# Performance work log

Measured on AMD Instinct MI355X. Metric: run time of the kernel, lower is better.

Reference implementation:

```python
import jax, jax.numpy as jnp
import numpy as np

B, S, D, H = 2, 2048, 1024, 16
DK = D // H


def setup_inputs() -> dict:
    key = jax.random.key(0)
    ks = jax.random.split(key, 9)
    s = 1.0 / np.sqrt(D)
    return {
        "x": jax.random.normal(ks[0], (B, S, D), dtype=jnp.float32),
        "wq": jax.random.normal(ks[1], (D, D), dtype=jnp.float32) * s,
        "bq": jax.random.normal(ks[2], (D,), dtype=jnp.float32) * 0.01,
        "wk": jax.random.normal(ks[3], (D, D), dtype=jnp.float32) * s,
        "bk": jax.random.normal(ks[4], (D,), dtype=jnp.float32) * 0.01,
        "wv": jax.random.normal(ks[5], (D, D), dtype=jnp.float32) * s,
        "bv": jax.random.normal(ks[6], (D,), dtype=jnp.float32) * 0.01,
        "wo": jax.random.normal(ks[7], (D, D), dtype=jnp.float32) * s,
        "bo": jax.random.normal(ks[8], (D,), dtype=jnp.float32) * 0.01,
    }


def reference(x, wq, bq, wk, bk, wv, bv, wo, bo):
    b, s, d = x.shape
    # Linear layers use torch convention: y = x @ W.T + b
    def proj(w, bias):
        y = jnp.einsum("bsd,ed->bse", x, w) + bias
        return y.reshape(b, s, H, DK).transpose(0, 2, 1, 3)  # (B,H,S,DK)

    q = proj(wq, bq)
    k = proj(wk, bk)
    v = proj(wv, bv)

    # Because each Q-chunk attends to the full K/V with m initialized to -inf,
    # the chunked online-softmax loop is exactly full softmax attention.
    scores = jnp.einsum("bhqd,bhkd->bhqk", q, k) / jnp.sqrt(jnp.float32(DK))
    attn = jax.nn.softmax(scores, axis=-1)
    out = jnp.einsum("bhqk,bhkd->bhqd", attn, v)  # (B,H,S,DK)

    out = out.transpose(0, 2, 1, 3).reshape(b, s, d)
    return jnp.einsum("bsd,ed->bse", out, wo) + bo
```

## Files before the change

### kernel.cpp

```cpp
#include <hip/hip_runtime.h>

typedef __attribute__((ext_vector_type(8))) short s16x8;
typedef __attribute__((ext_vector_type(4))) short s16x4;
typedef __attribute__((ext_vector_type(4))) float f32x4;

#define DEVI static __device__ __forceinline__

DEVI short f2bf(float f) {
  union { float f; unsigned u; } v; v.f = f;
  unsigned u = v.u;
  unsigned r = u + 0x7FFFu + ((u >> 16) & 1u);
  return (short)(r >> 16);
}
DEVI short f2bf_fast(float f) {
  union { float f; unsigned u; } v; v.f = f;
  return (short)((v.u + 0x8000u) >> 16);
}
DEVI float bf2f(short s) {
  union { unsigned u; float f; } v;
  v.u = ((unsigned)(unsigned short)s) << 16;
  return v.f;
}
DEVI f32x4 mfma16(s16x8 a, s16x8 b, f32x4 c) {
  return __builtin_amdgcn_mfma_f32_16x16x32_bf16(a, b, c, 0, 0, 0);
}
DEVI float fexp2(float x) {
#if __has_builtin(__builtin_amdgcn_exp2f)
  return __builtin_amdgcn_exp2f(x);
#else
  float r; asm("v_exp_f32 %0, %1" : "=v"(r) : "v"(x)); return r;
#endif
}
DEVI void gld16(const void* g, void* l) {
  __builtin_amdgcn_global_load_lds(
      (const __attribute__((address_space(1))) void*)g,
      (__attribute__((address_space(3))) void*)l, 16, 0, 0);
}

constexpr int Sc = 2048, Dc = 1024, Hc = 16, DKc = 64;
constexpr int Mc = 4096;

__global__ void detect_ker(const unsigned short* __restrict__ x, int* __restrict__ flag) {
  __shared__ int cnt;
  if (threadIdx.x == 0) cnt = 0;
  __syncthreads();
  int c = 0;
  for (int i = threadIdx.x; i < 4096; i += 256) {
    int e = (x[i] >> 7) & 0xFF;
    if (e >= 140) c++;
  }
  atomicAdd(&cnt, c);
  __syncthreads();
  if (threadIdx.x == 0) *flag = (cnt > 64) ? 1 : 0;
}

__global__ void norm_all(const void* x,
                         const void* w0, const void* w1, const void* w2, const void* w3,
                         const void* b0, const void* b1, const void* b2, const void* b3,
                         short* __restrict__ xdst, short* __restrict__ wdst,
                         float* __restrict__ bdst, const int* __restrict__ flag) {
  const int f = *flag;
  const int blk = blockIdx.x, tid = threadIdx.x;
  if (blk < 8192) {
    if (!f) return;
    const void* src; short* dst; int i;
    if (blk < 4096) {
      i = blk * 256 + tid; src = x; dst = xdst;
    } else {
      int j = (blk - 4096) * 256 + tid;
      int region = j >> 18;
      const void* ws[4] = {w0, w1, w2, w3};
      src = ws[region]; dst = wdst + (size_t)region * 1048576;
      i = j & 262143;
    }
    f32x4 v = ((const f32x4*)src)[i];
    s16x4 o;
#pragma unroll
    for (int j2 = 0; j2 < 4; ++j2) o[j2] = f2bf(v[j2]);
    ((s16x4*)dst)[i] = o;
  } else {
    const void* bs[4] = {b0, b1, b2, b3};
#pragma unroll
    for (int j = 0; j < 16; ++j) {
      int i = tid + j * 256;
      int r = i >> 10, k = i & 1023;
      bdst[i] = f ? ((const float*)bs[r])[k] : bf2f(((const short*)bs[r])[k]);
    }
  }
}

template <int EPI>
__global__ __launch_bounds__(256, 2)
void gemm_bt(const short* __restrict__ Aorig, const short* __restrict__ Acvt,
             const short* __restrict__ W0, const short* __restrict__ W1,
             const short* __restrict__ W2, const short* __restrict__ Wcvt,
             const float* __restrict__ bias_c, short* __restrict__ outQKV,
             short* __restrict__ outV, void* __restrict__ outFinal,
             const int* __restrict__ flag) {
  constexpr int K = Dc, N = Dc;
  const int z = blockIdx.z;
  const int f = *flag;
  const short* A = f ? Acvt : Aorig;
  const short* Wor = (z == 0) ? W0 : (z == 1) ? W1 : W2;
  const short* W = f ? (Wcvt + (size_t)z * 1048576) : Wor;
  const float* bias = bias_c + (size_t)z * N;
  const float oscale = (EPI == 0 && z == 0) ? 0.125f * 1.44269504f : 1.0f;

  __shared__ short lA[128 * 64];
  __shared__ short lB[128 * 64];

  const int tid = threadIdx.x;
  const int lane = tid & 63, wave = tid >> 6;
  const int l16 = lane & 15, quad = lane >> 4;
  const int wm0 = (wave >> 1) * 64, wn0 = (wave & 1) * 64;
  const int m0 = blockIdx.y * 128, n0 = blockIdx.x * 128;
  const int lr = lane >> 3;
  const int cg = ((lane & 7) ^ lr) * 8;
  const int x7 = l16 & 7;

  f32x4 acc[4][4] = {};

  for (int k0 = 0; k0 < K; k0 += 64) {
    __syncthreads();
#pragma unroll
    for (int it = 0; it < 4; ++it) {
      int rbase = wave * 32 + it * 8;
      gld16(&A[(size_t)(m0 + rbase + lr) * K + k0 + cg], &lA[rbase * 64]);
      gld16(&W[(size_t)(n0 + rbase + lr) * K + k0 + cg], &lB[rbase * 64]);
    }
    __syncthreads();
#pragma unroll
    for (int ks = 0; ks < 2; ++ks) {
      const int sw = ((ks * 4 + quad) ^ x7) * 8;
      s16x8 af[4], bfr[4];
#pragma unroll
      for (int i = 0; i < 4; ++i) {
        af[i]  = *(const s16x8*)&lA[(wm0 + i * 16 + l16) * 64 + sw];
        bfr[i] = *(const s16x8*)&lB[(wn0 + i * 16 + l16) * 64 + sw];
      }
#pragma unroll
      for (int mi = 0; mi < 4; ++mi)
#pragma unroll
        for (int ni = 0; ni < 4; ++ni)
          acc[mi][ni] = mfma16(af[mi], bfr[ni], acc[mi][ni]);
    }
  }

  if constexpr (EPI == 0) {
    if (z == 2) {
#pragma unroll
      for (int ni = 0; ni < 4; ++ni) {
        int n = n0 + wn0 + ni * 16 + l16;
        float bv = bias[n];
        int h = (n >> 6) & 15, dk = n & 63;
#pragma unroll
        for (int mi = 0; mi < 4; ++mi) {
          int mbase = m0 + wm0 + mi * 16 + quad * 4;
          int bb = mbase >> 11, s = mbase & 2047;
          s16x4 pk;
#pragma unroll
          for (int r = 0; r < 4; ++r) pk[r] = f2bf(acc[mi][ni][r] + bv);
          *(s16x4*)&outV[(((size_t)(bb * Hc + h)) * DKc + dk) * Sc + s] = pk;
        }
      }
      return;
    }
#pragma unroll
    for (int ni = 0; ni < 4; ++ni) {
      int n = n0 + wn0 + ni * 16 + l16;
      float bv = bias[n];
#pragma unroll
      for (int mi = 0; mi < 4; ++mi) {
#pragma unroll
        for (int r = 0; r < 4; ++r) {
          int m = m0 + wm0 + mi * 16 + quad * 4 + r;
          float v = (acc[mi][ni][r] + bv) * oscale;
          int bb = m >> 11, s = m & 2047, h = n >> 6, dk = n & 63;
          size_t idx = ((((size_t)bb * Hc + h) * Sc) + s) * DKc + dk +
                       (size_t)z * Mc * N;
          outQKV[idx] = f2bf(v);
        }
      }
    }
  } else {
#pragma unroll
    for (int ni = 0; ni < 4; ++ni) {
      int n = n0 + wn0 + ni * 16 + l16;
      float bv = bias[n];
#pragma unroll
      for (int mi = 0; mi < 4; ++mi) {
#pragma unroll
        for (int r = 0; r < 4; ++r) {
          int m = m0 + wm0 + mi * 16 + quad * 4 + r;
          float v = acc[mi][ni][r] + bv;
          if (f) ((float*)outFinal)[(size_t)m * N + n] = v;
          else   ((short*)outFinal)[(size_t)m * N + n] = f2bf(v);
        }
      }
    }
  }
}

__global__ __launch_bounds__(512, 4)
void attn_ker(const short* __restrict__ Q, const short* __restrict__ Kg,
              const short* __restrict__ Vt, short* __restrict__ O) {
  __shared__ short lK[2][64 * 64];
  __shared__ short lV[2][64 * 64];
  __shared__ short lP[8][16][72];

  const int tid = threadIdx.x;
  const int lane = tid & 63, wave = tid >> 6;
  const int l16 = lane & 15, quad = lane >> 4;
  const int lr = lane >> 3;
  const int cg = ((lane & 7) ^ lr) * 8;
  const int x7 = l16 & 7;

  const int bh = blockIdx.x;
  const short* Qb = Q + (size_t)bh * Sc * DKc;
  const short* Kb = Kg + (size_t)bh * Sc * DKc;
  const short* Vb = Vt + (size_t)bh * DKc * Sc;

  const int q0 = blockIdx.y * 128 + wave * 16;

  s16x8 qf[2];
#pragma unroll
  for (int ks = 0; ks < 2; ++ks)
    qf[ks] = *(const s16x8*)&Qb[(size_t)(q0 + l16) * DKc + ks * 32 + quad * 8];

  s16x8 ones = {};
  if (l16 == 0) {
#pragma unroll
    for (int j = 0; j < 8; ++j) ones[j] = (short)0x3F80;
  }
  const f32x4 initC = {-24.f, -24.f, -24.f, -24.f};

  f32x4 oacc[4] = {};
  f32x4 oln = {};

#define STAGE(BUF, KB)                                                          \
  {                                                                             \
    int rbase = wave * 8;                                                       \
    gld16(&Kb[(size_t)((KB) + rbase + lr) * DKc + cg], &lK[BUF][rbase * 64]);   \
    gld16(&Vb[(size_t)(rbase + lr) * Sc + (KB) + cg], &lV[BUF][rbase * 64]);    \
  }

  STAGE(0, 0)

  for (int kt = 0; kt < Sc / 64; ++kt) {
    const int p = kt & 1;
    __syncthreads();
    if (kt + 1 < Sc / 64) STAGE(p ^ 1, (kt + 1) * 64)

    f32x4 sacc[4];
    {
      const int sw0 = (quad ^ x7) * 8;
      s16x8 kf[4];
#pragma unroll
      for (int ni = 0; ni < 4; ++ni)
        kf[ni] = *(const s16x8*)&lK[p][(ni * 16 + l16) * 64 + sw0];
#pragma unroll
      for (int ni = 0; ni < 4; ++ni)
        sacc[ni] = mfma16(qf[0], kf[ni], initC);
    }
    {
      const int sw1 = ((4 + quad) ^ x7) * 8;
      s16x8 kf[4];
#pragma unroll
      for (int ni = 0; ni < 4; ++ni)
        kf[ni] = *(const s16x8*)&lK[p][(ni * 16 + l16) * 64 + sw1];
#pragma unroll
      for (int ni = 0; ni < 4; ++ni)
        sacc[ni] = mfma16(qf[1], kf[ni], sacc[ni]);
    }

#pragma unroll
    for (int r = 0; r < 4; ++r) {
      int row = quad * 4 + r;
#pragma unroll
      for (int ni = 0; ni < 4; ++ni)
        lP[wave][row][ni * 16 + l16] = f2bf_fast(fexp2(sacc[ni][r]));
    }

    s16x8 vf[2][4];
#pragma unroll
    for (int ks = 0; ks < 2; ++ks) {
      const int sw = ((ks * 4 + quad) ^ x7) * 8;
#pragma unroll
      for (int ni = 0; ni < 4; ++ni)
        vf[ks][ni] = *(const s16x8*)&lV[p][(ni * 16 + l16) * 64 + sw];
    }

    __builtin_amdgcn_s_waitcnt(0xc07f);

    s16x8 pf[2];
#pragma unroll
    for (int ks = 0; ks < 2; ++ks)
      pf[ks] = *(const s16x8*)&lP[wave][l16][ks * 32 + quad * 8];

#pragma unroll
    for (int ks = 0; ks < 2; ++ks) {
#pragma unroll
      for (int ni = 0; ni < 4; ++ni)
        oacc[ni] = mfma16(pf[ks], vf[ks][ni], oacc[ni]);
      oln = mfma16(pf[ks], ones, oln);
    }
  }
#undef STAGE

  const int bb = bh >> 4, h = bh & 15;
#pragma unroll
  for (int r = 0; r < 4; ++r) {
    float l = __shfl(oln[r], lane & 48);
    float inv = 1.0f / l;
    int srow = q0 + quad * 4 + r;
#pragma unroll
    for (int ni = 0; ni < 4; ++ni) {
      int col = h * DKc + ni * 16 + l16;
      O[((size_t)(bb * Sc + srow)) * Dc + col] = f2bf(oacc[ni][r] * inv);
    }
  }
}

extern "C" void kernel_launch(void* const* d_in, const int* in_sizes, int n_in,
                              void* d_out, int out_size, void* d_ws, size_t ws_size,
                              hipStream_t stream) {
  const void* x  = d_in[0];
  const void* wq = d_in[1]; const void* bq = d_in[2];
  const void* wk = d_in[3]; const void* bk = d_in[4];
  const void* wv = d_in[5]; const void* bv = d_in[6];
  const void* wo = d_in[7]; const void* bo = d_in[8];

  char* wsb = (char*)d_ws;
  int*   flag = (int*)wsb;
  short* x_c  = (short*)(wsb + 1024);
  short* w_c  = x_c + (size_t)4 * 1024 * 1024;
  float* b_c  = (float*)(wsb + 1024 + 16 * 1024 * 1024);
  short* Qc   = (short*)(wsb + 1024 + 16 * 1024 * 1024 + 16384);
  short* Kc   = Qc + (size_t)4 * 1024 * 1024;
  short* Vtc  = Kc + (size_t)4 * 1024 * 1024;
  short* Oc   = Vtc + (size_t)4 * 1024 * 1024;

  detect_ker<<<1, 256, 0, stream>>>((const unsigned short*)x, flag);

  norm_all<<<8193, 256, 0, stream>>>(x, wq, wk, wv, wo, bq, bk, bv, bo,
                                     x_c, w_c, b_c, flag);

  gemm_bt<0><<<dim3(8, 32, 3), 256, 0, stream>>>(
      (const short*)x, x_c,
      (const short*)wq, (const short*)wk, (const short*)wv, w_c,
      b_c, Qc, Vtc, nullptr, flag);

  attn_ker<<<dim3(32, 16), 512, 0, stream>>>(Qc, Kc, Vtc, Oc);

  gemm_bt<1><<<dim3(8, 32, 1), 256, 0, stream>>>(
      Oc, Oc,
      (const short*)wo, (const short*)wo, (const short*)wo, w_c + 3 * 1048576,
      b_c + 3 * 1024, nullptr, nullptr, d_out, flag);
}
```

Measured before the change: 204.8 us.

## Keep attention probabilities in registers via shuffles, shrink attn and out-proj tiles

The attention kernel now computes S^T (K as the A operand) so that exp'd probabilities can be packed to bf16 pairs and redistributed with lane shuffles into the PV MFMA operand layout. This removes the per-wave LDS round trip for P and its waitcnt. The attention block is halved to 4 waves with 64 queries each, doubling the grid. The output projection gets its own 64x64-tile GEMM, giving 1024 blocks instead of 256 for better CU fill. The risks are added shuffle and select overhead and less K/V reuse per block.

Result: no change. 205.0 us (+0.1%).

```diff
diff --git a/kernel.cpp b/kernel.cpp
--- a/kernel.cpp
+++ b/kernel.cpp
@@ -11,10 +11,6 @@
   unsigned u = v.u;
   unsigned r = u + 0x7FFFu + ((u >> 16) & 1u);
   return (short)(r >> 16);
-}
-DEVI short f2bf_fast(float f) {
-  union { float f; unsigned u; } v; v.f = f;
-  return (short)((v.u + 0x8000u) >> 16);
 }
 DEVI float bf2f(short s) {
   union { unsigned u; float f; } v;
@@ -30,6 +26,10 @@
 #else
   float r; asm("v_exp_f32 %0, %1" : "=v"(r) : "v"(x)); return r;
 #endif
+}
+DEVI unsigned packbf(float lo, float hi) {
+  union { float f; unsigned u; } a, b; a.f = lo; b.f = hi;
+  return __builtin_amdgcn_perm(b.u + 0x8000u, a.u + 0x8000u, 0x07060302u);
 }
 DEVI void gld16(const void* g, void* l) {
   __builtin_amdgcn_global_load_lds(
@@ -89,14 +89,12 @@
   }
 }
 
-template <int EPI>
 __global__ __launch_bounds__(256, 2)
-void gemm_bt(const short* __restrict__ Aorig, const short* __restrict__ Acvt,
-             const short* __restrict__ W0, const short* __restrict__ W1,
-             const short* __restrict__ W2, const short* __restrict__ Wcvt,
-             const float* __restrict__ bias_c, short* __restrict__ outQKV,
-             short* __restrict__ outV, void* __restrict__ outFinal,
-             const int* __restrict__ flag) {
+void gemm_qkv(const short* __restrict__ Aorig, const short* __restrict__ Acvt,
+              const short* __restrict__ W0, const short* __restrict__ W1,
+              const short* __restrict__ W2, const short* __restrict__ Wcvt,
+              const float* __restrict__ bias_c, short* __restrict__ outQKV,
+              short* __restrict__ outV, const int* __restrict__ flag) {
   constexpr int K = Dc, N = Dc;
   const int z = blockIdx.z;
   const int f = *flag;
@@ -104,7 +102,7 @@
   const short* Wor = (z == 0) ? W0 : (z == 1) ? W1 : W2;
   const short* W = f ? (Wcvt + (size_t)z * 1048576) : Wor;
   const float* bias = bias_c + (size_t)z * N;
-  const float oscale = (EPI == 0 && z == 0) ? 0.125f * 1.44269504f : 1.0f;
+  const float oscale = (z == 0) ? 0.125f * 1.44269504f : 1.0f;
 
   __shared__ short lA[128 * 64];
   __shared__ short lB[128 * 64];
@@ -146,67 +144,53 @@
     }
   }
 
-  if constexpr (EPI == 0) {
-    if (z == 2) {
-#pragma unroll
-      for (int ni = 0; ni < 4; ++ni) {
-        int n = n0 + wn0 + ni * 16 + l16;
-        float bv = bias[n];
-        int h = (n >> 6) & 15, dk = n & 63;
-#pragma unroll
-        for (int mi = 0; mi < 4; ++mi) {
-          int mbase = m0 + wm0 + mi * 16 + quad * 4;
-          int bb = mbase >> 11, s = mbase & 2047;
-          s16x4 pk;
-#pragma unroll
-          for (int r = 0; r < 4; ++r) pk[r] = f2bf(acc[mi][ni][r] + bv);
-          *(s16x4*)&outV[(((size_t)(bb * Hc + h)) * DKc + dk) * Sc + s] = pk;
-        }
-      }
-      return;
-    }
+  if (z == 2) {
 #pragma unroll
     for (int ni = 0; ni < 4; ++ni) {
       int n = n0 + wn0 + ni * 16 + l16;
       float bv = bias[n];
+      int h = (n >> 6) & 15, dk = n & 63;
 #pragma unroll
       for (int mi = 0; mi < 4; ++mi) {
-#pragma unroll
-        for (int r = 0; r < 4; ++r) {
-          int m = m0 + wm0 + mi * 16 + quad * 4 + r;
-          float v = (acc[mi][ni][r] + bv) * oscale;
-          int bb = m >> 11, s = m & 2047, h = n >> 6, dk = n & 63;
-          size_t idx = ((((size_t)bb * Hc + h) * Sc) + s) * DKc + dk +
-                       (size_t)z * Mc * N;
-          outQKV[idx] = f2bf(v);
-        }
+        int mbase = m0 + wm0 + mi * 16 + quad * 4;
+        int bb = mbase >> 11, s = mbase & 2047;
+        s16x4 pk;
+#pragma unroll
+        for (int r = 0; r < 4; ++r) pk[r] = f2bf(acc[mi][ni][r] + bv);
+        *(s16x4*)&outV[(((size_t)(bb * Hc + h)) * DKc + dk) * Sc + s] = pk;
       }
     }
-  } else {
-#pragma unroll
-    for (int ni = 0; ni < 4; ++ni) {
-      int n = n0 + wn0 + ni * 16 + l16;
-      float bv = bias[n];
-#pragma unroll
-      for (int mi = 0; mi < 4; ++mi) {
-#pragma unroll
-        for (int r = 0; r < 4; ++r) {
-          int m = m0 + wm0 + mi * 16 + quad * 4 + r;
-          float v = acc[mi][ni][r] + bv;
-          if (f) ((float*)outFinal)[(size_t)m * N + n] = v;
-          else   ((short*)outFinal)[(size_t)m * N + n] = f2bf(v);
-        }
+    return;
+  }
+#pragma unroll
+  for (int ni = 0; ni < 4; ++ni) {
+    int n = n0 + wn0 + ni * 16 + l16;
+    float bv = bias[n];
+#pragma unroll
+    for (int mi = 0; mi < 4; ++mi) {
+#pragma unroll
+      for (int r = 0; r < 4; ++r) {
+        int m = m0 + wm0 + mi * 16 + quad * 4 + r;
+        float v = (acc[mi][ni][r] + bv) * oscale;
+        int bb = m >> 11, s = m & 2047, h = n >> 6, dk = n & 63;
+        size_t idx = ((((size_t)bb * Hc + h) * Sc) + s) * DKc + dk +
+                     (size_t)z * Mc * N;
+        outQKV[idx] = f2bf(v);
       }
     }
   }
 }
 
-__global__ __launch_bounds__(512, 4)
-void attn_ker(const short* __restrict__ Q, const short* __restrict__ Kg,
-              const short* __restrict__ Vt, short* __restrict__ O) {
-  __shared__ short lK[2][64 * 64];
-  __shared__ short lV[2][64 * 64];
-  __shared__ short lP[8][16][72];
+__global__ __launch_bounds__(256, 4)
+void gemm_out(const short* __restrict__ A, const short* __restrict__ Worig,
+              const short* __restrict__ Wcvt, const float* __restrict__ bias,
+              void* __restrict__ out, const int* __restrict__ flag) {
+  constexpr int K = Dc, N = Dc;
+  const int f = *flag;
+  const short* W = f ? Wcvt : Worig;
+
+  __shared__ short lA[64 * 64];
+  __shared__ short lB[64 * 64];
 
   const int tid = threadIdx.x;
   const int lane = tid & 63, wave = tid >> 6;
@@ -214,13 +198,73 @@
   const int lr = lane >> 3;
   const int cg = ((lane & 7) ^ lr) * 8;
   const int x7 = l16 & 7;
+  const int wm0 = (wave >> 1) * 32, wn0 = (wave & 1) * 32;
+  const int m0 = blockIdx.y * 64, n0 = blockIdx.x * 64;
+
+  f32x4 acc[2][2] = {};
+
+  for (int k0 = 0; k0 < K; k0 += 64) {
+    __syncthreads();
+#pragma unroll
+    for (int it = 0; it < 2; ++it) {
+      int rbase = wave * 16 + it * 8;
+      gld16(&A[(size_t)(m0 + rbase + lr) * K + k0 + cg], &lA[rbase * 64]);
+      gld16(&W[(size_t)(n0 + rbase + lr) * K + k0 + cg], &lB[rbase * 64]);
+    }
+    __syncthreads();
+#pragma unroll
+    for (int ks = 0; ks < 2; ++ks) {
+      const int sw = ((ks * 4 + quad) ^ x7) * 8;
+      s16x8 af[2], bfr[2];
+#pragma unroll
+      for (int i = 0; i < 2; ++i) {
+        af[i]  = *(const s16x8*)&lA[(wm0 + i * 16 + l16) * 64 + sw];
+        bfr[i] = *(const s16x8*)&lB[(wn0 + i * 16 + l16) * 64 + sw];
+      }
+#pragma unroll
+      for (int mi = 0; mi < 2; ++mi)
+#pragma unroll
+        for (int ni = 0; ni < 2; ++ni)
+          acc[mi][ni] = mfma16(af[mi], bfr[ni], acc[mi][ni]);
+    }
+  }
+
+#pragma unroll
+  for (int ni = 0; ni < 2; ++ni) {
+    int n = n0 + wn0 + ni * 16 + l16;
+    float bv = bias[n];
+#pragma unroll
+    for (int mi = 0; mi < 2; ++mi) {
+#pragma unroll
+      for (int r = 0; r < 4; ++r) {
+        int m = m0 + wm0 + mi * 16 + quad * 4 + r;
+        float v = acc[mi][ni][r] + bv;
+        if (f) ((float*)out)[(size_t)m * N + n] = v;
+        else   ((short*)out)[(size_t)m * N + n] = f2bf(v);
+      }
+    }
+  }
+}
+
+__global__ __launch_bounds__(256, 4)
+void attn_ker(const short* __restrict__ Q, const short* __restrict__ Kg,
+              const short* __restrict__ Vt, short* __restrict__ O) {
+  __shared__ short lK[2][64 * 64];
+  __shared__ short lV[2][64 * 64];
+
+  const int tid = threadIdx.x;
+  const int lane = tid & 63, wave = tid >> 6;
+  const int l16 = lane & 15, quad = lane >> 4;
+  const int lr = lane >> 3;
+  const int cg = ((lane & 7) ^ lr) * 8;
+  const int x7 = l16 & 7;
 
   const int bh = blockIdx.x;
   const short* Qb = Q + (size_t)bh * Sc * DKc;
   const short* Kb = Kg + (size_t)bh * Sc * DKc;
   const short* Vb = Vt + (size_t)bh * DKc * Sc;
 
-  const int q0 = blockIdx.y * 128 + wave * 16;
+  const int q0 = blockIdx.y * 64 + wave * 16;
 
   s16x8 qf[2];
 #pragma unroll
@@ -234,14 +278,21 @@
   }
   const f32x4 initC = {-24.f, -24.f, -24.f, -24.f};
 
+  const int srcA = ((quad & 1) << 5) + l16;
+  const int srcB = srcA + 16;
+  const bool hisel = quad >= 2;
+
   f32x4 oacc[4] = {};
   f32x4 oln = {};
 
 #define STAGE(BUF, KB)                                                          \
   {                                                                             \
-    int rbase = wave * 8;                                                       \
-    gld16(&Kb[(size_t)((KB) + rbase + lr) * DKc + cg], &lK[BUF][rbase * 64]);   \
-    gld16(&Vb[(size_t)(rbase + lr) * Sc + (KB) + cg], &lV[BUF][rbase * 64]);    \
+    _Pragma("unroll")                                                           \
+    for (int it = 0; it < 2; ++it) {                                            \
+      int rbase = wave * 16 + it * 8;                                           \
+      gld16(&Kb[(size_t)((KB) + rbase + lr) * DKc + cg], &lK[BUF][rbase * 64]); \
+      gld16(&Vb[(size_t)(rbase + lr) * Sc + (KB) + cg], &lV[BUF][rbase * 64]);  \
+    }                                                                           \
   }
 
   STAGE(0, 0)
@@ -256,53 +307,57 @@
       const int sw0 = (quad ^ x7) * 8;
       s16x8 kf[4];
 #pragma unroll
-      for (int ni = 0; ni < 4; ++ni)
-        kf[ni] = *(const s16x8*)&lK[p][(ni * 16 + l16) * 64 + sw0];
-#pragma unroll
-      for (int ni = 0; ni < 4; ++ni)
-        sacc[ni] = mfma16(qf[0], kf[ni], initC);
+      for (int mi = 0; mi < 4; ++mi)
+        kf[mi] = *(const s16x8*)&lK[p][(mi * 16 + l16) * 64 + sw0];
+#pragma unroll
+      for (int mi = 0; mi < 4; ++mi)
+        sacc[mi] = mfma16(kf[mi], qf[0], initC);
     }
     {
       const int sw1 = ((4 + quad) ^ x7) * 8;
       s16x8 kf[4];
 #pragma unroll
-      for (int ni = 0; ni < 4; ++ni)
-        kf[ni] = *(const s16x8*)&lK[p][(ni * 16 + l16) * 64 + sw1];
-#pragma unroll
-      for (int ni = 0; ni < 4; ++ni)
-        sacc[ni] = mfma16(qf[1], kf[ni], sacc[ni]);
-    }
-
-#pragma unroll
-    for (int r = 0; r < 4; ++r) {
-      int row = quad * 4 + r;
-#pragma unroll
-      for (int ni = 0; ni < 4; ++ni)
-        lP[wave][row][ni * 16 + l16] = f2bf_fast(fexp2(sacc[ni][r]));
-    }
-
-    s16x8 vf[2][4];
+      for (int mi = 0; mi < 4; ++mi)
+        kf[mi] = *(const s16x8*)&lK[p][(mi * 16 + l16) * 64 + sw1];
+#pragma unroll
+      for (int mi = 0; mi < 4; ++mi)
+        sacc[mi] = mfma16(kf[mi], qf[1], sacc[mi]);
+    }
+
+    unsigned pk01[4], pk23[4];
+#pragma unroll
+    for (int mi = 0; mi < 4; ++mi) {
+      pk01[mi] = packbf(fexp2(sacc[mi][0]), fexp2(sacc[mi][1]));
+      pk23[mi] = packbf(fexp2(sacc[mi][2]), fexp2(sacc[mi][3]));
+    }
+
 #pragma unroll
     for (int ks = 0; ks < 2; ++ks) {
       const int sw = ((ks * 4 + quad) ^ x7) * 8;
+      s16x8 vf[4];
 #pragma unroll
       for (int ni = 0; ni < 4; ++ni)
-        vf[ks][ni] = *(const s16x8*)&lV[p][(ni * 16 + l16) * 64 + sw];
-    }
-
-    __builtin_amdgcn_s_waitcnt(0xc07f);
-
-    s16x8 pf[2];
-#pragma unroll
-    for (int ks = 0; ks < 2; ++ks)
-      pf[ks] = *(const s16x8*)&lP[wave][l16][ks * 32 + quad * 8];
-
-#pragma unroll
-    for (int ks = 0; ks < 2; ++ks) {
+        vf[ni] = *(const s16x8*)&lV[p][(ni * 16 + l16) * 64 + sw];
+
+      unsigned a0l = (unsigned)__shfl((int)pk01[ks * 2], srcA);
+      unsigned a0h = (unsigned)__shfl((int)pk01[ks * 2 + 1], srcA);
+      unsigned a1l = (unsigned)__shfl((int)pk23[ks * 2], srcA);
+      unsigned a1h = (unsigned)__shfl((int)pk23[ks * 2 + 1], srcA);
+      unsigned a2l = (unsigned)__shfl((int)pk01[ks * 2], srcB);
+      unsigned a2h = (unsigned)__shfl((int)pk01[ks * 2 + 1], srcB);
+      unsigned a3l = (unsigned)__shfl((int)pk23[ks * 2], srcB);
+      unsigned a3h = (unsigned)__shfl((int)pk23[ks * 2 + 1], srcB);
+      union { unsigned u[4]; s16x8 v; } pu;
+      pu.u[0] = hisel ? a0h : a0l;
+      pu.u[1] = hisel ? a1h : a1l;
+      pu.u[2] = hisel ? a2h : a2l;
+      pu.u[3] = hisel ? a3h : a3l;
+      s16x8 pf = pu.v;
+
 #pragma unroll
       for (int ni = 0; ni < 4; ++ni)
-        oacc[ni] = mfma16(pf[ks], vf[ks][ni], oacc[ni]);
-      oln = mfma16(pf[ks], ones, oln);
+        oacc[ni] = mfma16(pf, vf[ni], oacc[ni]);
+      oln = mfma16(pf, ones, oln);
     }
   }
 #undef STAGE
@@ -345,15 +400,13 @@
   norm_all<<<8193, 256, 0, stream>>>(x, wq, wk, wv, wo, bq, bk, bv, bo,
                                      x_c, w_c, b_c, flag);
 
-  gemm_bt<0><<<dim3(8, 32, 3), 256, 0, stream>>>(
+  gemm_qkv<<<dim3(8, 32, 3), 256, 0, stream>>>(
       (const short*)x, x_c,
       (const short*)wq, (const short*)wk, (const short*)wv, w_c,
-      b_c, Qc, Vtc, nullptr, flag);
-
-  attn_ker<<<dim3(32, 16), 512, 0, stream>>>(Qc, Kc, Vtc, Oc);
-
-  gemm_bt<1><<<dim3(8, 32, 1), 256, 0, stream>>>(
-      Oc, Oc,
-      (const short*)wo, (const short*)wo, (const short*)wo, w_c + 3 * 1048576,
-      b_c + 3 * 1024, nullptr, nullptr, d_out, flag);
-}
+      b_c, Qc, Vtc, flag);
+
+  attn_ker<<<dim3(32, 32), 256, 0, stream>>>(Qc, Kc, Vtc, Oc);
+
+  gemm_out<<<dim3(16, 64), 256, 0, stream>>>(
+      Oc, (const short*)wo, w_c + 3 * 1048576, b_c + 3 * 1024, d_out, flag);
+}
```
